# Kernel optimization log

Measured on AMD Instinct MI355X. Metric: run time of the kernel, lower is better.

Reference implementation:

```python
import jax, jax.numpy as jnp
import numpy as np

EPS = 1e-5

def _conv1x1(x, w, b):
    # x: [B,C,H,W], w: [O,C], b: [O]  (1x1 conv == channel matmul)
    return jnp.einsum('bchw,oc->bohw', x, w) + b[None, :, None, None]

def _bn_relu(y, gamma, beta, mean, var):
    inv = gamma / jnp.sqrt(var + EPS)
    return jax.nn.relu(y * inv[None, :, None, None] + (beta - mean * inv)[None, :, None, None])

def setup_inputs() -> dict:
    key = jax.random.key(0)
    ks = jax.random.split(key, 8)
    B, C, H, W = 8, 2048, 48, 48
    mid = C // 4  # k = 4 -> mid_ch = 512
    s_in = (2.0 / C) ** 0.5   # kaiming-like scale for 1x1 convs from C channels
    s_mid = (2.0 / mid) ** 0.5
    return {
        'x': jax.random.normal(ks[0], (B, C, H, W), jnp.float32),
        'f_w': jax.random.normal(ks[1], (mid, C), jnp.float32) * s_in,
        'f_b': jnp.zeros((mid,), jnp.float32),
        'f_gamma': jnp.ones((mid,), jnp.float32),
        'f_beta': jnp.zeros((mid,), jnp.float32),
        'f_mean': jnp.zeros((mid,), jnp.float32),
        'f_var': jnp.ones((mid,), jnp.float32),
        'g_w': jax.random.normal(ks[2], (mid, C), jnp.float32) * s_in,
        'g_b': jnp.zeros((mid,), jnp.float32),
        'g_gamma': jnp.ones((mid,), jnp.float32),
        'g_beta': jnp.zeros((mid,), jnp.float32),
        'g_mean': jnp.zeros((mid,), jnp.float32),
        'g_var': jnp.ones((mid,), jnp.float32),
        'h_w': jax.random.normal(ks[3], (mid, C), jnp.float32) * s_in,
        'h_b': jnp.zeros((mid,), jnp.float32),
        'v_w': jax.random.normal(ks[4], (C, mid), jnp.float32) * s_mid,
        'v_b': jnp.zeros((C,), jnp.float32),
    }

def reference(x, f_w, f_b, f_gamma, f_beta, f_mean, f_var,
              g_w, g_b, g_gamma, g_beta, g_mean, g_var,
              h_w, h_b, v_w, v_b):
    B, C, H, W = x.shape
    mid = f_w.shape[0]
    N = H * W
    f_x = _bn_relu(_conv1x1(x, f_w, f_b), f_gamma, f_beta, f_mean, f_var).reshape(B, mid, N)
    g_x = _bn_relu(_conv1x1(x, g_w, g_b), g_gamma, g_beta, g_mean, g_var).reshape(B, mid, N)
    h_x = _conv1x1(x, h_w, h_b).reshape(B, mid, N)
    # z = f_x^T @ g_x : [B, N, N]
    scores = jnp.einsum('bcn,bcm->bnm', f_x, g_x) * (mid ** -0.5)
    attn = jax.nn.softmax(scores, axis=-1)
    # z = attn @ h_x^T : [B, N, mid] -> [B, mid, H, W]
    z = jnp.einsum('bnm,bcm->bcn', attn, h_x).reshape(B, mid, H, W)
    z = jnp.einsum('bchw,oc->bohw', z, v_w) + v_b[None, :, None, None]
    return (z + x, attn)
```

## Files before the change

### kernel.cpp

```cpp
#include <hip/hip_runtime.h>
#include <math.h>

typedef unsigned short u16;
typedef unsigned short u16x8 __attribute__((ext_vector_type(8)));
typedef __bf16 bf16x8 __attribute__((ext_vector_type(8)));
typedef float f32x4 __attribute__((ext_vector_type(4)));

typedef __attribute__((address_space(1))) const unsigned int gu32;
typedef __attribute__((address_space(3))) unsigned int su32;

#define B_ 8
#define C_ 2048
#define MID_ 512
#define N_ 2304

#define BAR() do { asm volatile("" ::: "memory"); __builtin_amdgcn_s_barrier(); asm volatile("" ::: "memory"); } while (0)

#define QMFMA(AV, BV, MO, NO)                                                             \
  { _Pragma("unroll") for (int mfi = 0; mfi < 4; ++mfi) {                                 \
      _Pragma("unroll") for (int nfi = 0; nfi < 2; ++nfi) {                               \
        acc[MO + mfi][NO + nfi] = __builtin_amdgcn_mfma_f32_16x16x32_bf16(                \
            AV[0][mfi], BV[0][nfi], acc[MO + mfi][NO + nfi], 0, 0, 0);                    \
        acc[MO + mfi][NO + nfi] = __builtin_amdgcn_mfma_f32_16x16x32_bf16(                \
            AV[1][mfi], BV[1][nfi], acc[MO + mfi][NO + nfi], 0, 0, 0); } } }

static __device__ __forceinline__ u16 f2bf(float f) {
  union { float f; unsigned u; } c; c.f = f;
  unsigned u = c.u;
  u += 0x7fffu + ((u >> 16) & 1u);
  return (u16)(u >> 16);
}
static __device__ __forceinline__ float bf2f(u16 x) {
  union { unsigned u; float f; } c; c.u = ((unsigned)x) << 16; return c.f;
}

__global__ __launch_bounds__(256) void prep_wall_k(
    const float* __restrict__ fw, const float* __restrict__ gw,
    const float* __restrict__ hw, u16* __restrict__ wall) {
  int idx = blockIdx.x * 256 + threadIdx.x;
  if (idx >= 1536 * 2048) return;
  int r = idx >> 11;
  float v = (r < 512) ? fw[idx] : (r < 1024) ? gw[idx - (512 << 11)] : hw[idx - (1024 << 11)];
  wall[idx] = f2bf(v);
}

__global__ __launch_bounds__(256) void prep_vw_k(const float* __restrict__ vw, u16* __restrict__ o) {
  int idx = blockIdx.x * 256 + threadIdx.x;
  if (idx < 2048 * 512) o[idx] = f2bf(vw[idx]);
}

__global__ __launch_bounds__(256) void prep_sb_k(
    const float* fb, const float* fg, const float* fbe, const float* fm, const float* fv,
    const float* gb, const float* gg, const float* gbe, const float* gm, const float* gv,
    const float* hb, float* __restrict__ scale, float* __restrict__ bias) {
  int i = blockIdx.x * 256 + threadIdx.x;
  if (i >= 1536) return;
  if (i < 512) {
    float inv = fg[i] / sqrtf(fv[i] + 1e-5f);
    scale[i] = inv; bias[i] = fb[i] * inv + fbe[i] - fm[i] * inv;
  } else if (i < 1024) {
    int j = i - 512;
    float inv = gg[j] / sqrtf(gv[j] + 1e-5f);
    scale[i] = inv; bias[i] = gb[j] * inv + gbe[j] - gm[j] * inv;
  } else {
    scale[i] = 1.0f; bias[i] = hb[i - 1024];
  }
}

__global__ __launch_bounds__(256) void transpose_x_k(const float* __restrict__ x, u16* __restrict__ xT) {
  __shared__ float tile[64][68];
  const int b = blockIdx.z;
  const int n0 = blockIdx.x * 64, c0 = blockIdx.y * 64;
  const float* xb = x + (size_t)b * C_ * N_;
  u16* xTb = xT + (size_t)b * N_ * C_;
  const int r = threadIdx.x >> 2, q = threadIdx.x & 3;
  #pragma unroll
  for (int j = 0; j < 4; ++j) {
    float4 v = *(const float4*)&xb[(size_t)(c0 + r) * N_ + n0 + (q + 4 * j) * 4];
    *(float4*)&tile[r][(q + 4 * j) * 4] = v;
  }
  __syncthreads();
  #pragma unroll
  for (int g = 0; g < 2; ++g) {
    const int cl = (q * 2 + g) * 8;
    u16x8 w;
    #pragma unroll
    for (int e = 0; e < 8; ++e) w[e] = f2bf(tile[cl + e][r]);
    *(u16x8*)&xTb[(size_t)(n0 + r) * C_ + c0 + cl] = w;
  }
}

__global__ __launch_bounds__(256) void transpose_h_k(const u16* __restrict__ fghT, u16* __restrict__ hx) {
  __shared__ u16 tile[32][33];
  const int b = blockIdx.z;
  const int n0 = blockIdx.x * 32, c0 = blockIdx.y * 32;
  const u16* src = fghT + (size_t)b * N_ * 1536;
  u16* dst = hx + (size_t)b * MID_ * N_;
  const int tx = threadIdx.x & 31, ty = threadIdx.x >> 5;
  #pragma unroll
  for (int i = 0; i < 4; ++i)
    tile[ty + i * 8][tx] = src[(size_t)(n0 + ty + i * 8) * 1536 + 1024 + c0 + tx];
  __syncthreads();
  #pragma unroll
  for (int i = 0; i < 4; ++i)
    dst[(size_t)(c0 + ty + i * 8) * N_ + n0 + tx] = tile[tx][ty + i * 8];
}

#define EP_FG 0
#define EP_SCALE16 1
#define EP_FINAL 2

template<int EPI>
__global__ __launch_bounds__(512, 2) void gemm4_kernel(
    const u16* __restrict__ Ag, int lda, long long sA,
    const u16* __restrict__ Bg, int ldb, long long sB,
    void* __restrict__ Cg, int ldc, long long sC, int K,
    const float* __restrict__ ep_scale, const float* __restrict__ ep_bias,
    const float* __restrict__ ep_x, long long sX, float fscale)
{
  extern __shared__ __align__(16) u16 smem[];
  u16* As = smem;
  u16* Bs = smem + 2 * 256 * 64;

  const int tid = threadIdx.x;
  const int lane = tid & 63;
  const int wv = tid >> 6;
  const int b = blockIdx.z;
  const int m0 = blockIdx.y * 256;
  const int n0 = blockIdx.x * 256;
  const int wm = (wv >> 2) * 128;
  const int wn = (wv & 3) * 64;
  const int lr = lane & 15, lg = lane >> 4;

  const u16* Ab = Ag + (size_t)b * sA;
  const u16* Bb = Bg + (size_t)b * sB;
  const int nk = K >> 6;

  const int srow = lane >> 3;
  const int sksw = ((lane & 7) ^ srow) * 8;

  const int rdsw0 = ((0 + lg) ^ (lr & 7)) * 8;
  const int rdsw1 = ((4 + lg) ^ (lr & 7)) * 8;

  f32x4 acc[8][4];
  #pragma unroll
  for (int i = 0; i < 8; ++i)
    #pragma unroll
    for (int j = 0; j < 4; ++j)
      acc[i][j] = f32x4{0.f, 0.f, 0.f, 0.f};

  auto STAGE_A = [&](int p2, int t) {
    #pragma unroll
    for (int j = 0; j < 4; ++j) {
      const int rb = j * 64 + wv * 8;
      const u16* g = Ab + (size_t)(m0 + rb + srow) * lda + t * 64 + sksw;
      __builtin_amdgcn_global_load_lds((gu32*)g, (su32*)(As + p2 * 16384 + rb * 64), 16, 0, 0);
    }
  };
  auto STAGE_B = [&](int p2, int t) {
    #pragma unroll
    for (int j = 0; j < 4; ++j) {
      const int rb = j * 64 + wv * 8;
      const u16* g = Bb + (size_t)(n0 + rb + srow) * ldb + t * 64 + sksw;
      __builtin_amdgcn_global_load_lds((gu32*)g, (su32*)(Bs + p2 * 16384 + rb * 64), 16, 0, 0);
    }
  };

  STAGE_A(0, 0); STAGE_B(0, 0);
  if (nk > 1) { STAGE_A(1, 1); STAGE_B(1, 1); }

  for (int kt = 0; kt < nk; ++kt) {
    const int p = kt & 1;
    if (kt + 1 < nk) asm volatile("s_waitcnt vmcnt(8)" ::: "memory");
    else             asm volatile("s_waitcnt vmcnt(0)" ::: "memory");
    BAR();

    const u16* Asl = As + p * 16384;
    const u16* Bsl = Bs + p * 16384;
    const bool st = (kt + 2) < nk;
    const int ps = (kt + 2) & 1;

    bf16x8 aV[2][4], bLo[2][2], bHi[2][2];

    #pragma unroll
    for (int ks = 0; ks < 2; ++ks) {
      const int ro = ks ? rdsw1 : rdsw0;
      #pragma unroll
      for (int i = 0; i < 4; ++i)
        aV[ks][i] = *(const bf16x8*)(Asl + (wm + i * 16 + lr) * 64 + ro);
      #pragma unroll
      for (int i = 0; i < 2; ++i)
        bLo[ks][i] = *(const bf16x8*)(Bsl + (wn + i * 16 + lr) * 64 + ro);
    }
    BAR();
    __builtin_amdgcn_s_setprio(1);
    QMFMA(aV, bLo, 0, 0);
    __builtin_amdgcn_s_setprio(0);
    BAR();

    #pragma unroll
    for (int ks = 0; ks < 2; ++ks) {
      const int ro = ks ? rdsw1 : rdsw0;
      #pragma unroll
      for (int i = 0; i < 2; ++i)
        bHi[ks][i] = *(const bf16x8*)(Bsl + (wn + 32 + i * 16 + lr) * 64 + ro);
    }
    BAR();
    __builtin_amdgcn_s_setprio(1);
    QMFMA(aV, bHi, 0, 2);
    __builtin_amdgcn_s_setprio(0);
    BAR();

    #pragma unroll
    for (int ks = 0; ks < 2; ++ks) {
      const int ro = ks ? rdsw1 : rdsw0;
      #pragma unroll
      for (int i = 0; i < 4; ++i)
        aV[ks][i] = *(const bf16x8*)(Asl + (wm + 64 + i * 16 + lr) * 64 + ro);
    }
    if (st) STAGE_B(ps, kt + 2);
    BAR();
    __builtin_amdgcn_s_setprio(1);
    QMFMA(aV, bLo, 4, 0);
    __builtin_amdgcn_s_setprio(0);
    BAR();

    if (st) STAGE_A(ps, kt + 2);
    BAR();
    __builtin_amdgcn_s_setprio(1);
    QMFMA(aV, bHi, 4, 2);
    __builtin_amdgcn_s_setprio(0);
    BAR();
  }

  u16*   C16 = (u16*)Cg + (size_t)b * sC;
  float* C32 = (float*)Cg + (size_t)b * sC;
  const float* xb = (EPI == EP_FINAL) ? (ep_x + (size_t)b * sX) : nullptr;
  #pragma unroll
  for (int mf = 0; mf < 8; ++mf) {
    #pragma unroll
    for (int nf = 0; nf < 4; ++nf) {
      #pragma unroll
      for (int r = 0; r < 4; ++r) {
        int row = m0 + wm + mf * 16 + lg * 4 + r;
        int col = n0 + wn + nf * 16 + lr;
        float v = acc[mf][nf][r];
        if constexpr (EPI == EP_FG) {
          v = v * ep_scale[col] + ep_bias[col];
          if (col < 1024) v = fmaxf(v, 0.f);
          C16[(size_t)row * ldc + col] = f2bf(v);
        } else if constexpr (EPI == EP_SCALE16) {
          C16[(size_t)row * ldc + col] = f2bf(v * fscale);
        } else {
          v += ep_bias[row] + xb[(size_t)row * ldc + col];
          C32[(size_t)row * ldc + col] = v;
        }
      }
    }
  }
}

__global__ __launch_bounds__(256) void softmax_k(u16* __restrict__ SP, float* __restrict__ attn) {
  u16* sp = SP + (size_t)blockIdx.x * N_;
  float* ar = attn + (size_t)blockIdx.x * N_;
  const int tid = threadIdx.x;
  u16x8 s8 = *(const u16x8*)&sp[tid * 8];
  u16 st = sp[2048 + tid];
  float w[8], wt = bf2f(st);
  #pragma unroll
  for (int j = 0; j < 8; ++j) w[j] = bf2f(s8[j]);
  float mx = wt;
  #pragma unroll
  for (int j = 0; j < 8; ++j) mx = fmaxf(mx, w[j]);
  #pragma unroll
  for (int o = 32; o; o >>= 1) mx = fmaxf(mx, __shfl_xor(mx, o));
  __shared__ float red[4], red2[4];
  if ((tid & 63) == 0) red[tid >> 6] = mx;
  __syncthreads();
  mx = fmaxf(fmaxf(red[0], red[1]), fmaxf(red[2], red[3]));
  float s = 0.f;
  #pragma unroll
  for (int j = 0; j < 8; ++j) { w[j] = __expf(w[j] - mx); s += w[j]; }
  wt = __expf(wt - mx); s += wt;
  #pragma unroll
  for (int o = 32; o; o >>= 1) s += __shfl_xor(s, o);
  if ((tid & 63) == 0) red2[tid >> 6] = s;
  __syncthreads();
  s = red2[0] + red2[1] + red2[2] + red2[3];
  float inv = 1.0f / s;
  #pragma unroll
  for (int j = 0; j < 8; ++j) w[j] *= inv;
  wt *= inv;
  float4 o0 = {w[0], w[1], w[2], w[3]}, o1 = {w[4], w[5], w[6], w[7]};
  *(float4*)&ar[tid * 8] = o0;
  *(float4*)&ar[tid * 8 + 4] = o1;
  ar[2048 + tid] = wt;
  u16x8 p8;
  #pragma unroll
  for (int j = 0; j < 8; ++j) p8[j] = f2bf(w[j]);
  *(u16x8*)&sp[tid * 8] = p8;
  sp[2048 + tid] = f2bf(wt);
}

extern "C" void kernel_launch(void* const* d_in, const int* in_sizes, int n_in,
                              void* d_out, int out_size, void* d_ws, size_t ws_size,
                              hipStream_t stream) {
  const float* x    = (const float*)d_in[0];
  const float* f_w  = (const float*)d_in[1];
  const float* f_b  = (const float*)d_in[2];
  const float* f_ga = (const float*)d_in[3];
  const float* f_be = (const float*)d_in[4];
  const float* f_me = (const float*)d_in[5];
  const float* f_va = (const float*)d_in[6];
  const float* g_w  = (const float*)d_in[7];
  const float* g_b  = (const float*)d_in[8];
  const float* g_ga = (const float*)d_in[9];
  const float* g_be = (const float*)d_in[10];
  const float* g_me = (const float*)d_in[11];
  const float* g_va = (const float*)d_in[12];
  const float* h_w  = (const float*)d_in[13];
  const float* h_b  = (const float*)d_in[14];
  const float* v_w  = (const float*)d_in[15];
  const float* v_b  = (const float*)d_in[16];

  float* out0 = (float*)d_out;
  float* attn = out0 + (size_t)B_ * C_ * N_;

  char* p = (char*)d_ws;
  u16* xT   = (u16*)p; p += (size_t)B_ * N_ * C_ * 2;
  u16* fghT = (u16*)p; p += (size_t)B_ * N_ * 1536 * 2;
  u16* hx   = (u16*)p; p += (size_t)B_ * MID_ * N_ * 2;
  u16* ZT   = (u16*)p; p += (size_t)B_ * N_ * MID_ * 2;
  u16* Wall = (u16*)p; p += (size_t)1536 * C_ * 2;
  u16* vwb  = (u16*)p; p += (size_t)C_ * MID_ * 2;
  float* sc = (float*)p; p += 1536 * 4;
  float* bi = (float*)p; p += 1536 * 4;
  u16* SP   = (u16*)p; p += (size_t)B_ * N_ * N_ * 2;

  hipFuncSetAttribute((const void*)gemm4_kernel<EP_FG>,      hipFuncAttributeMaxDynamicSharedMemorySize, 131072);
  hipFuncSetAttribute((const void*)gemm4_kernel<EP_SCALE16>, hipFuncAttributeMaxDynamicSharedMemorySize, 131072);
  hipFuncSetAttribute((const void*)gemm4_kernel<EP_FINAL>,   hipFuncAttributeMaxDynamicSharedMemorySize, 131072);

  prep_wall_k<<<(1536 * 2048 + 255) / 256, 256, 0, stream>>>(f_w, g_w, h_w, Wall);
  prep_vw_k<<<(2048 * 512 + 255) / 256, 256, 0, stream>>>(v_w, vwb);
  prep_sb_k<<<6, 256, 0, stream>>>(f_b, f_ga, f_be, f_me, f_va,
                                   g_b, g_ga, g_be, g_me, g_va, h_b, sc, bi);
  transpose_x_k<<<dim3(N_ / 64, C_ / 64, B_), 256, 0, stream>>>(x, xT);

  gemm4_kernel<EP_FG><<<dim3(1536 / 256, N_ / 256, B_), 512, 131072, stream>>>(
      xT, C_, (long long)N_ * C_, Wall, C_, 0,
      fghT, 1536, (long long)N_ * 1536, C_, sc, bi, nullptr, 0, 0.f);

  transpose_h_k<<<dim3(N_ / 32, MID_ / 32, B_), 256, 0, stream>>>(fghT, hx);

  const float fscale = 0.044194173824159216f;
  gemm4_kernel<EP_SCALE16><<<dim3(N_ / 256, N_ / 256, B_), 512, 131072, stream>>>(
      fghT, 1536, (long long)N_ * 1536, fghT + 512, 1536, (long long)N_ * 1536,
      SP, N_, (long long)N_ * N_, MID_, nullptr, nullptr, nullptr, 0, fscale);

  softmax_k<<<B_ * N_, 256, 0, stream>>>(SP, attn);

  gemm4_kernel<EP_SCALE16><<<dim3(MID_ / 256, N_ / 256, B_), 512, 131072, stream>>>(
      SP, N_, (long long)N_ * N_, hx, N_, (long long)MID_ * N_,
      ZT, MID_, (long long)N_ * MID_, N_, nullptr, nullptr, nullptr, 0, 1.0f);

  gemm4_kernel<EP_FINAL><<<dim3(N_ / 256, C_ / 256, B_), 512, 131072, stream>>>(
      vwb, MID_, 0, ZT, MID_, (long long)N_ * MID_,
      out0, N_, (long long)C_ * N_, MID_, nullptr, v_b, x, (long long)C_ * N_, 0.f);
}
```

Before: 514.0 us.

## Remap GEMM tiles with XCD-aware swizzle and fold score scale into BN

```diff
diff --git a/kernel.cpp b/kernel.cpp
--- a/kernel.cpp
+++ b/kernel.cpp
@@ -55,9 +55,10 @@
     const float* hb, float* __restrict__ scale, float* __restrict__ bias) {
   int i = blockIdx.x * 256 + threadIdx.x;
   if (i >= 1536) return;
+  const float FS = 0.044194173824159216f;
   if (i < 512) {
     float inv = fg[i] / sqrtf(fv[i] + 1e-5f);
-    scale[i] = inv; bias[i] = fb[i] * inv + fbe[i] - fm[i] * inv;
+    scale[i] = inv * FS; bias[i] = (fb[i] * inv + fbe[i] - fm[i] * inv) * FS;
   } else if (i < 1024) {
     int j = i - 512;
     float inv = gg[j] / sqrtf(gv[j] + 1e-5f);
@@ -110,24 +111,42 @@
 #define EP_SCALE16 1
 #define EP_FINAL 2
 
-template<int EPI>
-__global__ __launch_bounds__(512, 2) void gemm4_kernel(
+template<int EPI, int SWZ, int GX, int GY>
+__global__ __launch_bounds__(512, 2) void gemm5_kernel(
     const u16* __restrict__ Ag, int lda, long long sA,
     const u16* __restrict__ Bg, int ldb, long long sB,
     void* __restrict__ Cg, int ldc, long long sC, int K,
     const float* __restrict__ ep_scale, const float* __restrict__ ep_bias,
-    const float* __restrict__ ep_x, long long sX, float fscale)
+    const float* __restrict__ ep_x, long long sX)
 {
   extern __shared__ __align__(16) u16 smem[];
   u16* As = smem;
   u16* Bs = smem + 2 * 256 * 64;
 
+  int tx, ty, tz;
+  {
+    const int L = blockIdx.x;
+    const int xcd = L & 7, r = L >> 3;
+    if constexpr (SWZ == 0) {
+      const int i = r % GX, j = (r / GX) * 8 + xcd;
+      tx = i; ty = j % GY; tz = j / GY;
+    } else if constexpr (SWZ == 1) {
+      const int i = r % GY, j = (r / GY) * 8 + xcd;
+      ty = i; tx = j % GX; tz = j / GX;
+    } else {
+      const int i = r % 9, jg = (r / 9) * 8 + xcd;
+      const int bx = jg % (GX / 3), rem = jg / (GX / 3);
+      const int by = rem % (GY / 3); tz = rem / (GY / 3);
+      tx = bx * 3 + i % 3; ty = by * 3 + i / 3;
+    }
+  }
+
   const int tid = threadIdx.x;
   const int lane = tid & 63;
   const int wv = tid >> 6;
-  const int b = blockIdx.z;
-  const int m0 = blockIdx.y * 256;
-  const int n0 = blockIdx.x * 256;
+  const int b = tz;
+  const int m0 = ty * 256;
+  const int n0 = tx * 256;
   const int wm = (wv >> 2) * 128;
   const int wn = (wv & 3) * 64;
   const int lr = lane & 15, lg = lane >> 4;
@@ -250,7 +269,7 @@
           if (col < 1024) v = fmaxf(v, 0.f);
           C16[(size_t)row * ldc + col] = f2bf(v);
         } else if constexpr (EPI == EP_SCALE16) {
-          C16[(size_t)row * ldc + col] = f2bf(v * fscale);
+          C16[(size_t)row * ldc + col] = f2bf(v);
         } else {
           v += ep_bias[row] + xb[(size_t)row * ldc + col];
           C32[(size_t)row * ldc + col] = v;
@@ -337,9 +356,10 @@
   float* bi = (float*)p; p += 1536 * 4;
   u16* SP   = (u16*)p; p += (size_t)B_ * N_ * N_ * 2;
 
-  hipFuncSetAttribute((const void*)gemm4_kernel<EP_FG>,      hipFuncAttributeMaxDynamicSharedMemorySize, 131072);
-  hipFuncSetAttribute((const void*)gemm4_kernel<EP_SCALE16>, hipFuncAttributeMaxDynamicSharedMemorySize, 131072);
-  hipFuncSetAttribute((const void*)gemm4_kernel<EP_FINAL>,   hipFuncAttributeMaxDynamicSharedMemorySize, 131072);
+  hipFuncSetAttribute((const void*)gemm5_kernel<EP_FG, 0, 6, 9>,      hipFuncAttributeMaxDynamicSharedMemorySize, 131072);
+  hipFuncSetAttribute((const void*)gemm5_kernel<EP_SCALE16, 2, 9, 9>, hipFuncAttributeMaxDynamicSharedMemorySize, 131072);
+  hipFuncSetAttribute((const void*)gemm5_kernel<EP_SCALE16, 0, 2, 9>, hipFuncAttributeMaxDynamicSharedMemorySize, 131072);
+  hipFuncSetAttribute((const void*)gemm5_kernel<EP_FINAL, 1, 9, 8>,   hipFuncAttributeMaxDynamicSharedMemorySize, 131072);
 
   prep_wall_k<<<(1536 * 2048 + 255) / 256, 256, 0, stream>>>(f_w, g_w, h_w, Wall);
   prep_vw_k<<<(2048 * 512 + 255) / 256, 256, 0, stream>>>(v_w, vwb);
@@ -347,24 +367,23 @@
                                    g_b, g_ga, g_be, g_me, g_va, h_b, sc, bi);
   transpose_x_k<<<dim3(N_ / 64, C_ / 64, B_), 256, 0, stream>>>(x, xT);
 
-  gemm4_kernel<EP_FG><<<dim3(1536 / 256, N_ / 256, B_), 512, 131072, stream>>>(
+  gemm5_kernel<EP_FG, 0, 6, 9><<<dim3(6 * 9 * 8), 512, 131072, stream>>>(
       xT, C_, (long long)N_ * C_, Wall, C_, 0,
-      fghT, 1536, (long long)N_ * 1536, C_, sc, bi, nullptr, 0, 0.f);
+      fghT, 1536, (long long)N_ * 1536, C_, sc, bi, nullptr, 0);
 
   transpose_h_k<<<dim3(N_ / 32, MID_ / 32, B_), 256, 0, stream>>>(fghT, hx);
 
-  const float fscale = 0.044194173824159216f;
-  gemm4_kernel<EP_SCALE16><<<dim3(N_ / 256, N_ / 256, B_), 512, 131072, stream>>>(
+  gemm5_kernel<EP_SCALE16, 2, 9, 9><<<dim3(9 * 9 * 8), 512, 131072, stream>>>(
       fghT, 1536, (long long)N_ * 1536, fghT + 512, 1536, (long long)N_ * 1536,
-      SP, N_, (long long)N_ * N_, MID_, nullptr, nullptr, nullptr, 0, fscale);
+      SP, N_, (long long)N_ * N_, MID_, nullptr, nullptr, nullptr, 0);
 
   softmax_k<<<B_ * N_, 256, 0, stream>>>(SP, attn);
 
-  gemm4_kernel<EP_SCALE16><<<dim3(MID_ / 256, N_ / 256, B_), 512, 131072, stream>>>(
+  gemm5_kernel<EP_SCALE16, 0, 2, 9><<<dim3(2 * 9 * 8), 512, 131072, stream>>>(
       SP, N_, (long long)N_ * N_, hx, N_, (long long)MID_ * N_,
-      ZT, MID_, (long long)N_ * MID_, N_, nullptr, nullptr, nullptr, 0, 1.0f);
-
-  gemm4_kernel<EP_FINAL><<<dim3(N_ / 256, C_ / 256, B_), 512, 131072, stream>>>(
+      ZT, MID_, (long long)N_ * MID_, N_, nullptr, nullptr, nullptr, 0);
+
+  gemm5_kernel<EP_FINAL, 1, 9, 8><<<dim3(9 * 8 * 8), 512, 131072, stream>>>(
       vwb, MID_, 0, ZT, MID_, (long long)N_ * MID_,
-      out0, N_, (long long)C_ * N_, MID_, nullptr, v_b, x, (long long)C_ * N_, 0.f);
-}
+      out0, N_, (long long)C_ * N_, MID_, nullptr, v_b, x, (long long)C_ * N_);
+}
```

Result: no change. 505.2 us (-1.7%).
